# Optimization experiments

Measured on AMD Instinct MI355X. Metric: run time of the kernel, lower is better.

The kernel has to match this reference:

```python
import jax, jax.numpy as jnp
import numpy as np

B, T, S_ENC, D = 2, 1024, 1024, 2048
NQ, NKV, H = 16, 8, 256
EPS = 1e-6
CAP = 50.0
SCALE = 0.0625  # query_pre_attn_scalar = head_dim**-0.5
BASE = 10000
K_MASK = -2.3819763e+38


def rms_norm(x, scale, eps=EPS):
    var = jnp.mean(jnp.square(x), axis=-1, keepdims=True)
    return x * jax.lax.rsqrt(var + eps) * (1.0 + scale)


def apply_rope(x, positions, base=BASE):
    # x: [B, L, N, H], positions: [B, L] float. rope_proportion=1.0 -> full head.
    head_dim = x.shape[-1]
    timescale = base ** (2.0 / head_dim * jnp.arange(head_dim // 2, dtype=jnp.float32))
    sinusoid = positions[..., None] / timescale  # [B, L, H/2]
    sinusoid = sinusoid[..., None, :]            # [B, L, 1, H/2]
    sin, cos = jnp.sin(sinusoid), jnp.cos(sinusoid)
    x1, x2 = jnp.split(x, 2, axis=-1)
    return jnp.concatenate([x1 * cos - x2 * sin, x2 * cos + x1 * sin], axis=-1).astype(x.dtype)


def setup_inputs() -> dict:
    key = jax.random.key(0)
    ks = jax.random.split(key, 6)
    hidden_states = jax.random.normal(ks[0], (B, T, D), jnp.float32)
    encoder_hidden_states = jax.random.normal(ks[1], (B, S_ENC, D), jnp.float32)
    position_ids = jnp.broadcast_to(jnp.arange(T, dtype=jnp.int32), (B, T))
    causal = jnp.tril(jnp.ones((T, T), bool))
    merged = jnp.concatenate([causal, jnp.ones((T, S_ENC), bool)], axis=-1)
    merged_attention_mask = jnp.broadcast_to(merged[None, None], (B, 1, T, T + S_ENC))
    q_w = jax.random.normal(ks[2], (NQ, D, H), jnp.float32) * 0.02
    k_w = jax.random.normal(ks[3], (NKV, D, H), jnp.float32) * 0.02
    v_w = jax.random.normal(ks[4], (NKV, D, H), jnp.float32) * 0.02
    o_w = jax.random.normal(ks[5], (NQ, H, D), jnp.float32) * 0.02
    q_scale = jnp.zeros((H,), jnp.float32)
    k_scale = jnp.zeros((H,), jnp.float32)
    return {
        'hidden_states': hidden_states,
        'encoder_hidden_states': encoder_hidden_states,
        'position_ids': position_ids,
        'merged_attention_mask': merged_attention_mask,
        'q_w': q_w, 'k_w': k_w, 'v_w': v_w, 'o_w': o_w,
        'q_scale': q_scale, 'k_scale': k_scale,
    }


def reference(hidden_states, encoder_hidden_states, position_ids, merged_attention_mask,
              q_w, k_w, v_w, o_w, q_scale, k_scale):
    # Fused QKV projections
    q = jnp.einsum('BTD,NDH->BTNH', hidden_states, q_w)
    self_k = jnp.einsum('BTD,NDH->BTNH', hidden_states, k_w)
    self_v = jnp.einsum('BTD,NDH->BTNH', hidden_states, v_w)
    # QK RMSNorm
    q = rms_norm(q, q_scale)
    self_k = rms_norm(self_k, k_scale)
    # RoPE on decoder-side q/k only
    pos = position_ids.astype(jnp.float32)
    q = apply_rope(q, pos)
    self_k = apply_rope(self_k, pos)
    # Cross KV (no RoPE, k-norm applied)
    cross_k = rms_norm(jnp.einsum('BTD,NDH->BTNH', encoder_hidden_states, k_w), k_scale)
    cross_v = jnp.einsum('BTD,NDH->BTNH', encoder_hidden_states, v_w)
    # Merge KV: [B, T+S_enc, NKV, H]
    k = jnp.concatenate([self_k, cross_k], axis=1)
    v = jnp.concatenate([self_v, cross_v], axis=1)
    q = q * SCALE
    # GQA: group query heads over kv heads
    G = NQ // NKV
    qg = q.reshape(B, T, NKV, G, H)
    logits = jnp.einsum('BTKGH,BSKH->BKGTS', qg, k)
    # Logit soft-cap
    logits = CAP * jnp.tanh(logits / CAP)
    mask = merged_attention_mask[:, 0][:, None, None]  # [B,1,1,T,S_comb]
    logits = jnp.where(mask, logits, K_MASK)
    probs = jax.nn.softmax(logits, axis=-1)
    out = jnp.einsum('BKGTS,BSKH->BTKGH', probs, v).reshape(B, T, NQ, H)
    return jnp.einsum('BTNH,NHD->BTD', out, o_w)
```

## Files before the change

kernel.cpp:

```cpp
#include <hip/hip_runtime.h>
#include <hip/hip_bf16.h>
#include <stdint.h>

typedef __hip_bfloat16 bf16;
typedef __attribute__((ext_vector_type(8))) short bv8;
typedef __attribute__((ext_vector_type(4))) float f32x4;


__device__ __forceinline__ f32x4 mfma16(bv8 a, bv8 b, f32x4 c) {
  return __builtin_amdgcn_mfma_f32_16x16x32_bf16(a, b, c, 0, 0, 0);
}

__device__ __forceinline__ void gload16(const void* g, void* lds) {
  __builtin_amdgcn_global_load_lds((const __attribute__((address_space(1))) void*)g,
                                   (__attribute__((address_space(3))) void*)lds, 16, 0, 0);
}

__device__ __forceinline__ void storeC(float* p, float v) { *p = v; }
__device__ __forceinline__ void storeC(bf16* p, float v) { *p = __float2bfloat16(v); }

__global__ void cast2_f32_bf16(const float* __restrict__ a, const float* __restrict__ b,
                               bf16* __restrict__ da, bf16* __restrict__ db, int n4each) {
  int i = blockIdx.x * blockDim.x + threadIdx.x;
  const float* s;
  bf16* d;
  if (i < n4each) { s = a; d = da; }
  else            { s = b; d = db; i -= n4each; }
  float4 v = reinterpret_cast<const float4*>(s)[i];
  bf16 t[4] = {__float2bfloat16(v.x), __float2bfloat16(v.y),
               __float2bfloat16(v.z), __float2bfloat16(v.w)};
  reinterpret_cast<uint64_t*>(d)[i] = *reinterpret_cast<uint64_t*>(t);
}

__global__ void transpose_all(const float* __restrict__ q_w, const float* __restrict__ k_w,
                              const float* __restrict__ v_w, const float* __restrict__ o_w,
                              bf16* __restrict__ wqkvt, bf16* __restrict__ owt) {
  __shared__ float tile[32][33];
  const int bid = blockIdx.x;
  const float* s;
  bf16* d;
  int R, C, c0, r0;
  if (bid < 16384) {
    const int z = bid >> 9;
    const int rem = bid & 511;
    s = (z < 16) ? q_w + (size_t)z * 524288
      : (z < 24) ? k_w + (size_t)(z - 16) * 524288
                 : v_w + (size_t)(z - 24) * 524288;
    d = wqkvt + (size_t)z * 524288;
    R = 2048; C = 256;
    c0 = (rem & 7) * 32; r0 = (rem >> 3) * 32;
  } else {
    const int rem = bid - 16384;
    s = o_w; d = owt;
    R = 4096; C = 2048;
    c0 = (rem & 63) * 32; r0 = (rem >> 6) * 32;
  }
  const int x = threadIdx.x, y = threadIdx.y;
#pragma unroll
  for (int i = 0; i < 32; i += 8)
    tile[y + i][x] = s[(size_t)(r0 + y + i) * C + c0 + x];
  __syncthreads();
#pragma unroll
  for (int i = 0; i < 32; i += 8)
    d[(size_t)(c0 + y + i) * R + r0 + x] = __float2bfloat16(tile[x][y + i]);
}

__global__ void transpose_v2(const bf16* __restrict__ vself, const bf16* __restrict__ vcross,
                             bf16* __restrict__ dst) {
  __shared__ bf16 tile[32][33];
  const int z = blockIdx.z;
  const int zz = z & 15, b = zz >> 3, kvh = zz & 7;
  const bool cross = z >= 16;
  const bf16* srcb = cross ? vcross : vself;
  const int src_ld = cross ? 4096 : 8192;
  const int t0 = cross ? 1024 : 0;
  const bf16* s = srcb + (size_t)(b * 1024) * src_ld + kvh * 256;
  bf16* d = dst + (size_t)(zz * 256) * 2048 + t0;
  const int h0 = blockIdx.x * 32, tt0 = blockIdx.y * 32;
  const int x = threadIdx.x, y = threadIdx.y;
#pragma unroll
  for (int i = 0; i < 32; i += 8)
    tile[y + i][x] = s[(size_t)(tt0 + y + i) * src_ld + h0 + x];
  __syncthreads();
#pragma unroll
  for (int i = 0; i < 32; i += 8)
    d[(size_t)(h0 + y + i) * 2048 + tt0 + x] = tile[x][y + i];
}

template <typename CT>
__device__ __forceinline__ void gemm_body(const bf16* __restrict__ A, const bf16* __restrict__ Bt,
                                          CT* __restrict__ C, int N, int K,
                                          int m0, int n0, int kbase, int ksteps) {
  __shared__ __align__(16) bf16 As[128 * 32];
  __shared__ __align__(16) bf16 Bs[128 * 32];
  const int tid = threadIdx.x;
  const int w = tid >> 6, l = tid & 63;
  const int wr = w >> 1, wc = w & 1;
  const int l15 = l & 15, lhi = l >> 4;
  const bf16* ag = A + (size_t)(m0 + (tid >> 2)) * K + kbase + (tid & 3) * 8;
  const bf16* bg = Bt + (size_t)(n0 + (tid >> 2)) * K + kbase + (tid & 3) * 8;
  bf16* asw = As + w * 512;
  bf16* bsw = Bs + w * 512;
  f32x4 acc[4][4] = {};
  for (int k0 = 0; k0 < ksteps; k0 += 32) {
    gload16(ag + k0, asw);
    gload16(ag + (size_t)64 * K + k0, asw + 2048);
    gload16(bg + k0, bsw);
    gload16(bg + (size_t)64 * K + k0, bsw + 2048);
    asm volatile("s_waitcnt vmcnt(0)" ::: "memory");
    __syncthreads();
    bv8 af[4], bfv[4];
#pragma unroll
    for (int m = 0; m < 4; ++m)
      af[m] = *reinterpret_cast<const bv8*>(As + (wr * 64 + m * 16 + l15) * 32 + lhi * 8);
#pragma unroll
    for (int n = 0; n < 4; ++n)
      bfv[n] = *reinterpret_cast<const bv8*>(Bs + (wc * 64 + n * 16 + l15) * 32 + lhi * 8);
#pragma unroll
    for (int m = 0; m < 4; ++m)
#pragma unroll
      for (int n = 0; n < 4; ++n)
        acc[m][n] = mfma16(af[m], bfv[n], acc[m][n]);
    __syncthreads();
  }
  const int r0 = m0 + wr * 64 + lhi * 4;
  const int c0 = n0 + wc * 64 + l15;
#pragma unroll
  for (int m = 0; m < 4; ++m)
#pragma unroll
    for (int n = 0; n < 4; ++n) {
      f32x4 v = acc[m][n];
#pragma unroll
      for (int j = 0; j < 4; ++j)
        storeC(&C[(size_t)(r0 + m * 16 + j) * N + c0 + n * 16], v[j]);
    }
}

__launch_bounds__(256)
__global__ void gemm_proj(const bf16* __restrict__ hid, const bf16* __restrict__ enc,
                          const bf16* __restrict__ wqkvt, bf16* __restrict__ cself,
                          bf16* __restrict__ ccross) {
  const int bx = blockIdx.x;
  const bool cross = bx >= 64;
  const bf16* A = cross ? enc : hid;
  const bf16* Bt = cross ? wqkvt + 8388608 : wqkvt;
  bf16* C = cross ? ccross : cself;
  const int N = cross ? 4096 : 8192;
  const int n0 = (cross ? bx - 64 : bx) * 128;
  gemm_body<bf16>(A, Bt, C, N, 2048, blockIdx.y * 128, n0, 0, 2048);
}

__launch_bounds__(256)
__global__ void gemm_osplit(const bf16* __restrict__ A, const bf16* __restrict__ Bt,
                            float* __restrict__ out, float* __restrict__ p1,
                            float* __restrict__ p2, float* __restrict__ p3) {
  const int z = blockIdx.z;
  float* C = (z == 0) ? out : (z == 1) ? p1 : (z == 2) ? p2 : p3;
  gemm_body<float>(A, Bt, C, 2048, 4096, blockIdx.y * 128, blockIdx.x * 128,
                   z * 1024, 1024);
}

__global__ void add_inplace4(float* __restrict__ out, const float* __restrict__ p1,
                             const float* __restrict__ p2, const float* __restrict__ p3,
                             int n4) {
  int i = blockIdx.x * blockDim.x + threadIdx.x;
  if (i >= n4) return;
  float4 a = reinterpret_cast<float4*>(out)[i];
  float4 b = reinterpret_cast<const float4*>(p1)[i];
  float4 c = reinterpret_cast<const float4*>(p2)[i];
  float4 d = reinterpret_cast<const float4*>(p3)[i];
  a.x += b.x + c.x + d.x;
  a.y += b.y + c.y + d.y;
  a.z += b.z + c.z + d.z;
  a.w += b.w + c.w + d.w;
  reinterpret_cast<float4*>(out)[i] = a;
}

__launch_bounds__(256)
__global__ void norm_all(const bf16* __restrict__ cself, const bf16* __restrict__ ccross,
                         const float* __restrict__ q_s, const float* __restrict__ k_s,
                         const int* __restrict__ pos_ids,
                         bf16* __restrict__ qb, bf16* __restrict__ kbuf) {
  const int rid = blockIdx.x * 4 + (threadIdx.x >> 6);
  const int l = threadIdx.x & 63;
  const bf16* src;
  const float* scale;
  bf16* dst;
  int r, src_ld, src_col0, nheads, dst_S, dst_t0;
  float mul;
  bool rope;
  if (rid < 32768) {
    r = rid; src = cself; src_ld = 8192; src_col0 = 0; scale = q_s;
    dst = qb; nheads = 16; dst_S = 1024; dst_t0 = 0; mul = 0.0625f; rope = true;
  } else if (rid < 49152) {
    r = rid - 32768; src = cself; src_ld = 8192; src_col0 = 4096; scale = k_s;
    dst = kbuf; nheads = 8; dst_S = 2048; dst_t0 = 0; mul = 1.0f; rope = true;
  } else {
    r = rid - 49152; src = ccross; src_ld = 4096; src_col0 = 0; scale = k_s;
    dst = kbuf; nheads = 8; dst_S = 2048; dst_t0 = 1024; mul = 1.0f; rope = false;
  }
  const int token = r / nheads;
  const int n = r - token * nheads;
  const int b = token >> 10;
  const int t = token & 1023;
  const size_t soff = (size_t)token * src_ld + src_col0 + n * 256 + l * 4;
  bf16 xb[4];
  *reinterpret_cast<uint64_t*>(xb) = *reinterpret_cast<const uint64_t*>(src + soff);
  float x[4];
#pragma unroll
  for (int c = 0; c < 4; ++c) x[c] = __bfloat162float(xb[c]);
  float ss = x[0] * x[0] + x[1] * x[1] + x[2] * x[2] + x[3] * x[3];
#pragma unroll
  for (int d = 1; d < 64; d <<= 1) ss += __shfl_xor(ss, d);
  const float rr = rsqrtf(ss * (1.0f / 256.0f) + 1e-6f);
  float v[4];
#pragma unroll
  for (int c = 0; c < 4; ++c) v[c] = x[c] * rr * (1.0f + scale[l * 4 + c]);
  if (rope) {
    const float pos = (float)pos_ids[token];
    float o[4];
#pragma unroll
    for (int c = 0; c < 4; ++c) {
      const int j = (l & 31) * 4 + c;
      const float inv_ts = exp2f(-(float)j * 0.10381025296523007f);
      const float arg = pos * inv_ts;
      const float sj = sinf(arg), cj = cosf(arg);
      const float partner = __shfl_xor(v[c], 32);
      o[c] = (l < 32) ? (v[c] * cj - partner * sj) : (v[c] * cj + partner * sj);
    }
#pragma unroll
    for (int c = 0; c < 4; ++c) v[c] = o[c];
  }
  bf16 ob[4];
#pragma unroll
  for (int c = 0; c < 4; ++c) ob[c] = __float2bfloat16(v[c] * mul);
  const size_t doff = ((size_t)((b * nheads + n) * dst_S + dst_t0 + t)) * 256 + l * 4;
  *reinterpret_cast<uint64_t*>(dst + doff) = *reinterpret_cast<uint64_t*>(ob);
}

__launch_bounds__(512, 2)
__global__ void attn_kernel(const bf16* __restrict__ qb, const bf16* __restrict__ kb,
                            const bf16* __restrict__ vt, bf16* __restrict__ attn_out) {
  __shared__ __align__(16) bf16 Ks[2][64 * 256];
  __shared__ __align__(16) bf16 Vs[2][256 * 64];
  __shared__ __align__(16) bf16 pbuf[2][64 * 72];
  __shared__ float rsb[2][2][2][2][4][4];
  const int lin = blockIdx.x + 16 * blockIdx.y;
  const int kvc = (lin & 7) | (((lin >> 7) & 1) << 3);
  const int qt  = (lin >> 3) & 15;
  const int b = kvc >> 3, kvh = kvc & 7;
  const int tid = threadIdx.x, w = tid >> 6, l = tid & 63;
  const int g = w >> 2, qsp = (w >> 1) & 1, sh = w & 1, hq = w & 3;
  const int n = kvh * 2 + g;
  const int l15 = l & 15, lhi = l >> 4;
  const int xr = (l15 & 7) << 4;

  const bf16* kbase = kb + (size_t)(b * 8 + kvh) * 2048 * 256;
  const bf16* vbase = vt + (size_t)(b * 8 + kvh) * 256 * 2048;

  const bf16* ksrc[4];
  const bf16* vsrc[4];
#pragma unroll
  for (int i = 0; i < 4; ++i) {
    const int r0 = (w * 4 + i) * 2 + (l >> 5);
    const int cbs = ((l & 31) * 16) ^ ((r0 & 7) << 4);
    ksrc[i] = kbase + r0 * 256 + (cbs >> 1);
    const int h0 = (w * 4 + i) * 8 + (l >> 3);
    const int cbv = ((l & 7) * 16) ^ ((h0 & 7) << 4);
    vsrc[i] = vbase + (size_t)h0 * 2048 + (cbv >> 1);
  }

  bv8 qf[2][8];
#pragma unroll
  for (int qs2 = 0; qs2 < 2; ++qs2) {
    const bf16* qp = qb + ((size_t)(b * 16 + n) * 1024 + qt * 64 +
                           (qsp * 2 + qs2) * 16 + l15) * 256 + lhi * 8;
#pragma unroll
    for (int f = 0; f < 8; ++f) qf[qs2][f] = *reinterpret_cast<const bv8*>(qp + f * 32);
  }

  f32x4 oacc[4][4] = {};
  float rs[2][4] = {};

  const int nt = qt + 17;

#pragma unroll
  for (int i = 0; i < 4; ++i) gload16(ksrc[i], &Ks[0][(w * 4 + i) * 512]);
#pragma unroll
  for (int i = 0; i < 4; ++i) gload16(vsrc[i], &Vs[0][(w * 4 + i) * 512]);
  asm volatile("s_waitcnt vmcnt(0)" ::: "memory");
  __syncthreads();

  for (int it = 0; it < nt; ++it) {
    const int cur = it & 1;
    if (it + 1 < nt) {
      const int itn = it + 1;
      const int s1 = (itn <= qt) ? itn * 64 : 1024 + (itn - qt - 1) * 64;
#pragma unroll
      for (int i = 0; i < 4; ++i)
        gload16(ksrc[i] + (size_t)s1 * 256, &Ks[cur ^ 1][(w * 4 + i) * 512]);
#pragma unroll
      for (int i = 0; i < 4; ++i)
        gload16(vsrc[i] + s1, &Vs[cur ^ 1][(w * 4 + i) * 512]);
    }
    f32x4 lacc[2][2] = {};
    __builtin_amdgcn_s_setprio(1);
#pragma unroll
    for (int ss2 = 0; ss2 < 2; ++ss2) {
      const int rbase = ((sh * 2 + ss2) * 16 + l15) * 256;
#pragma unroll
      for (int f = 0; f < 8; ++f) {
        const int off = rbase + (((f * 64 + lhi * 16) ^ xr) >> 1);
        bv8 kf = *reinterpret_cast<const bv8*>(&Ks[cur][off]);
        lacc[0][ss2] = mfma16(qf[0][f], kf, lacc[0][ss2]);
        lacc[1][ss2] = mfma16(qf[1][f], kf, lacc[1][ss2]);
      }
    }
    __builtin_amdgcn_s_setprio(0);
    const bool diag = (it == qt);
#pragma unroll
    for (int qs2 = 0; qs2 < 2; ++qs2)
#pragma unroll
      for (int ss2 = 0; ss2 < 2; ++ss2)
#pragma unroll
        for (int j = 0; j < 4; ++j) {
          const float raw = lacc[qs2][ss2][j];
          const float e2 = __expf(raw * 0.04f);
          const bool ok = !diag ||
              ((sh * 2 + ss2) * 16 + l15 <= (qsp * 2 + qs2) * 16 + lhi * 4 + j);
          const float p = ok ? __expf(50.f - __fdividef(100.f, e2 + 1.f)) : 0.f;
          rs[qs2][j] += p;
          pbuf[g][((qsp * 2 + qs2) * 16 + lhi * 4 + j) * 72 + (sh * 2 + ss2) * 16 + l15] =
              __float2bfloat16(p);
        }
    __syncthreads();
    __builtin_amdgcn_s_setprio(1);
#pragma unroll
    for (int ks = 0; ks < 2; ++ks) {
      bv8 pa[4];
#pragma unroll
      for (int qs = 0; qs < 4; ++qs)
        pa[qs] = *reinterpret_cast<const bv8*>(&pbuf[g][(qs * 16 + l15) * 72 + ks * 32 + lhi * 8]);
#pragma unroll
      for (int i = 0; i < 4; ++i) {
        const int off = ((hq * 4 + i) * 16 + l15) * 64 + (((ks * 64 + lhi * 16) ^ xr) >> 1);
        bv8 vf = *reinterpret_cast<const bv8*>(&Vs[cur][off]);
#pragma unroll
        for (int qs = 0; qs < 4; ++qs) oacc[qs][i] = mfma16(pa[qs], vf, oacc[qs][i]);
      }
    }
    __builtin_amdgcn_s_setprio(0);
    asm volatile("s_waitcnt vmcnt(0)" ::: "memory");
    __syncthreads();
  }
#pragma unroll
  for (int qs2 = 0; qs2 < 2; ++qs2)
#pragma unroll
    for (int j = 0; j < 4; ++j) {
      float s = rs[qs2][j];
      s += __shfl_xor(s, 1);
      s += __shfl_xor(s, 2);
      s += __shfl_xor(s, 4);
      s += __shfl_xor(s, 8);
      if (l15 == 0) rsb[g][qsp][sh][qs2][j][lhi] = s;
    }
  __syncthreads();
  float invr[4][4];
#pragma unroll
  for (int qs = 0; qs < 4; ++qs)
#pragma unroll
    for (int j = 0; j < 4; ++j)
      invr[qs][j] = 1.0f / (rsb[g][qs >> 1][0][qs & 1][j][lhi] +
                            rsb[g][qs >> 1][1][qs & 1][j][lhi]);
  bf16* op = attn_out + ((size_t)(b * 1024 + qt * 64 + lhi * 4) * 4096) + n * 256 + l15;
#pragma unroll
  for (int qs = 0; qs < 4; ++qs)
#pragma unroll
    for (int i = 0; i < 4; ++i)
#pragma unroll
      for (int j = 0; j < 4; ++j)
        op[(size_t)(qs * 16 + j) * 4096 + (hq * 4 + i) * 16] =
            __float2bfloat16(oacc[qs][i][j] * invr[qs][j]);
}

extern "C" void kernel_launch(void* const* d_in, const int* in_sizes, int n_in,
                              void* d_out, int out_size, void* d_ws, size_t ws_size,
                              hipStream_t stream) {
  (void)in_sizes; (void)n_in; (void)out_size; (void)ws_size;
  const float* hidden = (const float*)d_in[0];
  const float* enc    = (const float*)d_in[1];
  const int*   pos    = (const int*)d_in[2];
  const float* q_w = (const float*)d_in[4];
  const float* k_w = (const float*)d_in[5];
  const float* v_w = (const float*)d_in[6];
  const float* o_w = (const float*)d_in[7];
  const float* q_s = (const float*)d_in[8];
  const float* k_s = (const float*)d_in[9];
  float* out = (float*)d_out;

  char* base = (char*)d_ws;
  bf16* hid_b  = (bf16*)(base + 0);
  bf16* enc_b  = (bf16*)(base + 8388608);
  bf16* qb     = (bf16*)(base + 0);
  float* p2    = (float*)(base + 0);
  bf16* wqkvt  = (bf16*)(base + 16777216);
  bf16* kbuf   = (bf16*)(base + 16777216);
  float* p3    = (float*)(base + 16777216);
  bf16* vtb    = (bf16*)(base + 33554432);
  bf16* owt    = (bf16*)(base + 50331648);
  bf16* cself  = (bf16*)(base + 67108864);
  bf16* attn_b = (bf16*)(base + 67108864);
  float* p1    = (float*)(base + 83886080);
  bf16* ccross = (bf16*)(base + 100663296);

  dim3 tb32(32, 8);
  cast2_f32_bf16<<<8192, 256, 0, stream>>>(hidden, enc, hid_b, enc_b, 1048576);
  transpose_all<<<24576, tb32, 0, stream>>>(q_w, k_w, v_w, o_w, wqkvt, owt);
  gemm_proj<<<dim3(96, 16), 256, 0, stream>>>(hid_b, enc_b, wqkvt, cself, ccross);
  norm_all<<<16384, 256, 0, stream>>>(cself, ccross, q_s, k_s, pos, qb, kbuf);
  transpose_v2<<<dim3(8, 32, 32), tb32, 0, stream>>>(cself + 6144, ccross + 2048, vtb);
  attn_kernel<<<dim3(16, 16), 512, 0, stream>>>(qb, kbuf, vtb, attn_b);
  gemm_osplit<<<dim3(16, 16, 4), 256, 0, stream>>>(attn_b, owt, out, p1, p2, p3);
  add_inplace4<<<4096, 256, 0, stream>>>(out, p1, p2, p3, 1048576);
}
```

Baseline: 373.8 us.

## Balance causal attention by pairing light and heavy query row tiles per block

```diff
diff --git a/kernel.cpp b/kernel.cpp
--- a/kernel.cpp
+++ b/kernel.cpp
@@ -244,16 +244,21 @@
   __shared__ __align__(16) bf16 Ks[2][64 * 256];
   __shared__ __align__(16) bf16 Vs[2][256 * 64];
   __shared__ __align__(16) bf16 pbuf[2][64 * 72];
-  __shared__ float rsb[2][2][2][2][4][4];
+  __shared__ float rsb[2][4][2][4][4];
   const int lin = blockIdx.x + 16 * blockIdx.y;
   const int kvc = (lin & 7) | (((lin >> 7) & 1) << 3);
-  const int qt  = (lin >> 3) & 15;
+  const int p   = (lin >> 3) & 15;
   const int b = kvc >> 3, kvh = kvc & 7;
   const int tid = threadIdx.x, w = tid >> 6, l = tid & 63;
-  const int g = w >> 2, qsp = (w >> 1) & 1, sh = w & 1, hq = w & 3;
+  const int g = w >> 2, i2 = (w >> 1) & 1, sh = w & 1, hq = w & 3;
   const int n = kvh * 2 + g;
   const int l15 = l & 15, lhi = l >> 4;
   const int xr = (l15 & 7) << 4;
+
+  const int rA = p * 32, rB = (31 - p) * 32;
+  const int ntSelf = ((31 - p) >> 1) + 1;
+  const int nASelf = (p >> 1) + 1;
+  const int nt = ntSelf + 16;
 
   const bf16* kbase = kb + (size_t)(b * 8 + kvh) * 2048 * 256;
   const bf16* vbase = vt + (size_t)(b * 8 + kvh) * 256 * 2048;
@@ -272,17 +277,15 @@
 
   bv8 qf[2][8];
 #pragma unroll
-  for (int qs2 = 0; qs2 < 2; ++qs2) {
-    const bf16* qp = qb + ((size_t)(b * 16 + n) * 1024 + qt * 64 +
-                           (qsp * 2 + qs2) * 16 + l15) * 256 + lhi * 8;
-#pragma unroll
-    for (int f = 0; f < 8; ++f) qf[qs2][f] = *reinterpret_cast<const bv8*>(qp + f * 32);
+  for (int h = 0; h < 2; ++h) {
+    const int rbase = (h ? rB : rA) + i2 * 16;
+    const bf16* qp = qb + ((size_t)(b * 16 + n) * 1024 + rbase + l15) * 256 + lhi * 8;
+#pragma unroll
+    for (int f = 0; f < 8; ++f) qf[h][f] = *reinterpret_cast<const bv8*>(qp + f * 32);
   }
 
   f32x4 oacc[4][4] = {};
   float rs[2][4] = {};
-
-  const int nt = qt + 17;
 
 #pragma unroll
   for (int i = 0; i < 4; ++i) gload16(ksrc[i], &Ks[0][(w * 4 + i) * 512]);
@@ -293,9 +296,12 @@
 
   for (int it = 0; it < nt; ++it) {
     const int cur = it & 1;
+    const int s0 = (it < ntSelf) ? it * 64 : 1024 + (it - ntSelf) * 64;
+    const bool selfpart = it < ntSelf;
+    const bool aAct = (it < nASelf) || !selfpart;
     if (it + 1 < nt) {
       const int itn = it + 1;
-      const int s1 = (itn <= qt) ? itn * 64 : 1024 + (itn - qt - 1) * 64;
+      const int s1 = (itn < ntSelf) ? itn * 64 : 1024 + (itn - ntSelf) * 64;
 #pragma unroll
       for (int i = 0; i < 4; ++i)
         gload16(ksrc[i] + (size_t)s1 * 256, &Ks[cur ^ 1][(w * 4 + i) * 512]);
@@ -312,41 +318,55 @@
       for (int f = 0; f < 8; ++f) {
         const int off = rbase + (((f * 64 + lhi * 16) ^ xr) >> 1);
         bv8 kf = *reinterpret_cast<const bv8*>(&Ks[cur][off]);
-        lacc[0][ss2] = mfma16(qf[0][f], kf, lacc[0][ss2]);
         lacc[1][ss2] = mfma16(qf[1][f], kf, lacc[1][ss2]);
+        if (aAct) lacc[0][ss2] = mfma16(qf[0][f], kf, lacc[0][ss2]);
       }
     }
     __builtin_amdgcn_s_setprio(0);
-    const bool diag = (it == qt);
-#pragma unroll
-    for (int qs2 = 0; qs2 < 2; ++qs2)
+#pragma unroll
+    for (int h = 0; h < 2; ++h) {
+      if (h == 0 && !aAct) continue;
+      const int slot = h ? (i2 + 2) : i2;
+      const int rbase = (h ? rB : rA) + i2 * 16;
 #pragma unroll
       for (int ss2 = 0; ss2 < 2; ++ss2)
 #pragma unroll
         for (int j = 0; j < 4; ++j) {
-          const float raw = lacc[qs2][ss2][j];
+          const float raw = lacc[h][ss2][j];
           const float e2 = __expf(raw * 0.04f);
-          const bool ok = !diag ||
-              ((sh * 2 + ss2) * 16 + l15 <= (qsp * 2 + qs2) * 16 + lhi * 4 + j);
-          const float p = ok ? __expf(50.f - __fdividef(100.f, e2 + 1.f)) : 0.f;
-          rs[qs2][j] += p;
-          pbuf[g][((qsp * 2 + qs2) * 16 + lhi * 4 + j) * 72 + (sh * 2 + ss2) * 16 + l15] =
-              __float2bfloat16(p);
+          const int s_idx = s0 + (sh * 2 + ss2) * 16 + l15;
+          const int trow = rbase + lhi * 4 + j;
+          const bool ok = !selfpart || (s_idx <= trow);
+          const float pv = ok ? __expf(50.f - __fdividef(100.f, e2 + 1.f)) : 0.f;
+          rs[h][j] += pv;
+          pbuf[g][(slot * 16 + lhi * 4 + j) * 72 + (sh * 2 + ss2) * 16 + l15] =
+              __float2bfloat16(pv);
         }
+    }
     __syncthreads();
     __builtin_amdgcn_s_setprio(1);
 #pragma unroll
     for (int ks = 0; ks < 2; ++ks) {
-      bv8 pa[4];
-#pragma unroll
-      for (int qs = 0; qs < 4; ++qs)
-        pa[qs] = *reinterpret_cast<const bv8*>(&pbuf[g][(qs * 16 + l15) * 72 + ks * 32 + lhi * 8]);
+      bv8 paB[2], paA[2];
+#pragma unroll
+      for (int q = 0; q < 2; ++q)
+        paB[q] = *reinterpret_cast<const bv8*>(
+            &pbuf[g][((2 + q) * 16 + l15) * 72 + ks * 32 + lhi * 8]);
+      if (aAct)
+#pragma unroll
+        for (int q = 0; q < 2; ++q)
+          paA[q] = *reinterpret_cast<const bv8*>(
+              &pbuf[g][(q * 16 + l15) * 72 + ks * 32 + lhi * 8]);
 #pragma unroll
       for (int i = 0; i < 4; ++i) {
         const int off = ((hq * 4 + i) * 16 + l15) * 64 + (((ks * 64 + lhi * 16) ^ xr) >> 1);
         bv8 vf = *reinterpret_cast<const bv8*>(&Vs[cur][off]);
-#pragma unroll
-        for (int qs = 0; qs < 4; ++qs) oacc[qs][i] = mfma16(pa[qs], vf, oacc[qs][i]);
+        oacc[2][i] = mfma16(paB[0], vf, oacc[2][i]);
+        oacc[3][i] = mfma16(paB[1], vf, oacc[3][i]);
+        if (aAct) {
+          oacc[0][i] = mfma16(paA[0], vf, oacc[0][i]);
+          oacc[1][i] = mfma16(paA[1], vf, oacc[1][i]);
+        }
       }
     }
     __builtin_amdgcn_s_setprio(0);
@@ -354,33 +374,34 @@
     __syncthreads();
   }
 #pragma unroll
-  for (int qs2 = 0; qs2 < 2; ++qs2)
+  for (int h = 0; h < 2; ++h) {
+    const int slot = h ? (i2 + 2) : i2;
 #pragma unroll
     for (int j = 0; j < 4; ++j) {
-      float s = rs[qs2][j];
+      float s = rs[h][j];
       s += __shfl_xor(s, 1);
       s += __shfl_xor(s, 2);
       s += __shfl_xor(s, 4);
       s += __shfl_xor(s, 8);
-      if (l15 == 0) rsb[g][qsp][sh][qs2][j][lhi] = s;
-    }
+      if (l15 == 0) rsb[g][slot][sh][j][lhi] = s;
+    }
+  }
   __syncthreads();
-  float invr[4][4];
-#pragma unroll
-  for (int qs = 0; qs < 4; ++qs)
+  const int rowb[4] = {rA, rA + 16, rB, rB + 16};
+  bf16* op = attn_out + (size_t)(b * 1024) * 4096 + n * 256 + l15;
+#pragma unroll
+  for (int slot = 0; slot < 4; ++slot) {
+    float invr[4];
 #pragma unroll
     for (int j = 0; j < 4; ++j)
-      invr[qs][j] = 1.0f / (rsb[g][qs >> 1][0][qs & 1][j][lhi] +
-                            rsb[g][qs >> 1][1][qs & 1][j][lhi]);
-  bf16* op = attn_out + ((size_t)(b * 1024 + qt * 64 + lhi * 4) * 4096) + n * 256 + l15;
-#pragma unroll
-  for (int qs = 0; qs < 4; ++qs)
+      invr[j] = 1.0f / (rsb[g][slot][0][j][lhi] + rsb[g][slot][1][j][lhi]);
 #pragma unroll
     for (int i = 0; i < 4; ++i)
 #pragma unroll
       for (int j = 0; j < 4; ++j)
-        op[(size_t)(qs * 16 + j) * 4096 + (hq * 4 + i) * 16] =
-            __float2bfloat16(oacc[qs][i][j] * invr[qs][j]);
+        op[(size_t)(rowb[slot] + lhi * 4 + j) * 4096 + (hq * 4 + i) * 16] =
+            __float2bfloat16(oacc[slot][i][j] * invr[j]);
+  }
 }
 
 extern "C" void kernel_launch(void* const* d_in, const int* in_sizes, int n_in,
```

After: 367.5 us, median of 3. No clear change (-1.7%).
